# Kernel tuning notes

Measured on AMD Instinct MI355X. Metric: run time of the kernel, lower is better.

The kernel has to match this reference:

```python
import jax, jax.numpy as jnp
import numpy as np

SIZE = 4096
NB = 16            # nr_blocks_per_row
NDROP = 8          # nr_blocks_to_drop_per_row
BATCH = 8192
BLOCK = SIZE // NB # 256


def _block_mask():
    # latin_square(n): S[i,j] = ((i+j) mod n) + 1, values 1..n, each once per row/col
    i = np.arange(NB)
    S = ((i[:, None] + i[None, :]) % NB) + 1
    m = S > NDROP  # keep NB-NDROP blocks per row
    mask = np.repeat(np.repeat(m, BLOCK, axis=0), BLOCK, axis=1)
    return jnp.asarray(mask)  # [SIZE, SIZE] bool


def setup_inputs() -> dict:
    key = jax.random.key(0)
    kx, kw, kb = jax.random.split(key, 3)
    x = jax.random.normal(kx, (BATCH, SIZE), dtype=jnp.float32)
    # kaiming_normal_ default: fan_in mode, relu gain -> std = sqrt(2/fan_in)
    weight = jax.random.normal(kw, (SIZE, SIZE), dtype=jnp.float32) * jnp.sqrt(2.0 / SIZE)
    # uniform(-1,1) scaled by sqrt(1/size)
    bias = jax.random.uniform(kb, (SIZE,), minval=-1.0, maxval=1.0, dtype=jnp.float32) * jnp.sqrt(1.0 / SIZE)
    mask = _block_mask()
    return {"x": x, "weight": weight, "bias": bias, "mask": mask}


def reference(x, weight, bias, mask):
    # x @ (mask * weight).T + bias
    w = jnp.where(mask, weight, jnp.zeros((), dtype=weight.dtype))
    return x @ w.T + bias
```

## Files before the change

### kernel.cpp

```cpp
#include <hip/hip_runtime.h>
#include <hip/hip_bf16.h>
#include <stdint.h>


typedef __bf16 bf16x8 __attribute__((ext_vector_type(8)));
typedef float  f32x16 __attribute__((ext_vector_type(16)));

#define AS1 __attribute__((address_space(1)))
#define AS3 __attribute__((address_space(3)))

__device__ __forceinline__ void async_cp16(const void* g, void* l) {
  __builtin_amdgcn_global_load_lds((const AS1 void*)g, (AS3 void*)l, 16, 0, 0);
}

__device__ __forceinline__ uint32_t pack_bf16(float a, float b) {
  uint32_t ua = __float_as_uint(a);
  ua += 0x7fffu + ((ua >> 16) & 1u);
  uint32_t ub = __float_as_uint(b);
  ub += 0x7fffu + ((ub >> 16) & 1u);
  return (ua >> 16) | (ub & 0xffff0000u);
}

__global__ __launch_bounds__(256) void cvt_x(const float* __restrict__ x,
                                             uint2* __restrict__ xb) {
  const int t = threadIdx.x;
  const int b = blockIdx.x;
  const float4* p = (const float4*)(x + (size_t)b * 4096);
  uint2* o = xb + (size_t)b * 1024;
  float4 a0 = p[t];
  float4 a1 = p[t + 256];
  float4 a2 = p[t + 512];
  float4 a3 = p[t + 768];
  o[t]       = make_uint2(pack_bf16(a0.x, a0.y), pack_bf16(a0.z, a0.w));
  o[t + 256] = make_uint2(pack_bf16(a1.x, a1.y), pack_bf16(a1.z, a1.w));
  o[t + 512] = make_uint2(pack_bf16(a2.x, a2.y), pack_bf16(a2.z, a2.w));
  o[t + 768] = make_uint2(pack_bf16(a3.x, a3.y), pack_bf16(a3.z, a3.w));
}

__global__ __launch_bounds__(256) void cvt_w(const float* __restrict__ w,
                                             uint2* __restrict__ wb) {
  const int t = threadIdx.x;
  const int n = blockIdx.x;
  const int kstart = ((8 - (n >> 8)) & 15) << 8;
  const float* src = w + (size_t)n * 4096;
  uint2* dst = wb + (size_t)n * 512;
  float4 a0 = *(const float4*)(src + ((kstart + 4 * t) & 4095));
  float4 a1 = *(const float4*)(src + ((kstart + 1024 + 4 * t) & 4095));
  dst[t]       = make_uint2(pack_bf16(a0.x, a0.y), pack_bf16(a0.z, a0.w));
  dst[t + 256] = make_uint2(pack_bf16(a1.x, a1.y), pack_bf16(a1.z, a1.w));
}

__global__ __launch_bounds__(512, 2) void gemm_bs8(
    const uint16_t* __restrict__ X,
    const uint16_t* __restrict__ W,
    const float* __restrict__ bias,
    float* __restrict__ out) {
  __shared__ char L[131072];

  const int tid = threadIdx.x;
  const int lin = blockIdx.x;
  const int xcd = lin & 7;
  const int idx = lin >> 3;
  const int bm = idx >> 1;
  const int bn = (xcd << 1) + (idx & 1);
  const int m0 = bm << 8;
  const int n0 = bn << 8;
  const int kstart = ((8 - bn) & 15) << 8;

  const int trow = tid >> 3;
  const int chswz = (((tid & 7) ^ (trow & 7)) << 3);
  const uint16_t* Xa = X + (size_t)(m0 + trow) * 4096 + chswz;
  const uint16_t* Wa = W + (size_t)(n0 + trow) * 2048 + chswz;
  char* dA = L + tid * 16;
  char* dB = L + 32768 + tid * 16;

  auto stageA = [&](int buf, int s) {
    const int kb = (kstart + (s << 6)) & 4095;
    const uint16_t* p = Xa + kb;
    char* d = dA + (buf << 16);
#pragma unroll
    for (int c = 0; c < 4; ++c)
      async_cp16(p + (size_t)(c << 6) * 4096, d + (c << 13));
  };
  auto stageB = [&](int buf, int s) {
    const uint16_t* p = Wa + (s << 6);
    char* d = dB + (buf << 16);
#pragma unroll
    for (int c = 0; c < 4; ++c)
      async_cp16(p + (size_t)(c << 6) * 2048, d + (c << 13));
  };

  const int lane = tid & 63;
  const int wv = tid >> 6;
  const int wmh = wv >> 2;
  const int wnq = wv & 3;
  const int cl = lane & 31;
  const int g01 = lane >> 5;
  const int lx7 = lane & 7;
  int sl[4];
#pragma unroll
  for (int s = 0; s < 4; ++s) sl[s] = (((2 * s + g01) ^ lx7) << 4);
  const int aoff = (wmh * 128 + cl) * 128;
  const int boff = 32768 + (wnq * 64 + cl) * 128;

  f32x16 acc[4][2];
#pragma unroll
  for (int i = 0; i < 4; ++i)
#pragma unroll
    for (int j = 0; j < 2; ++j)
#pragma unroll
      for (int e = 0; e < 16; ++e) acc[i][j][e] = 0.f;

  bf16x8 av[4][4];
  bf16x8 bv[4];

#define VMW(N) asm volatile("s_waitcnt vmcnt(" #N ")" ::: "memory")

#define PHASE(BUFB, QN, DOA, WAITSTMT, STAGE)                                 \
  {                                                                           \
    if (DOA) {                                                                \
      _Pragma("unroll")                                                       \
      for (int i = 0; i < 4; ++i)                                             \
        _Pragma("unroll")                                                     \
        for (int s = 0; s < 4; ++s)                                           \
          av[i][s] = *(const bf16x8*)(L + (BUFB) + aoff + i * 4096 + sl[s]);  \
    }                                                                         \
    _Pragma("unroll")                                                         \
    for (int s = 0; s < 4; ++s)                                               \
      bv[s] = *(const bf16x8*)(L + (BUFB) + boff + (QN) * 4096 + sl[s]);      \
    STAGE;                                                                    \
    __builtin_amdgcn_s_barrier();                                             \
    asm volatile("s_waitcnt lgkmcnt(0)" ::: "memory");                        \
    __builtin_amdgcn_sched_barrier(0);                                        \
    __builtin_amdgcn_s_setprio(1);                                            \
    _Pragma("unroll")                                                         \
    for (int s = 0; s < 4; ++s)                                               \
      _Pragma("unroll")                                                       \
      for (int i = 0; i < 4; ++i)                                             \
        acc[i][QN] = __builtin_amdgcn_mfma_f32_32x32x16_bf16(                 \
            av[i][s], bv[s], acc[i][QN], 0, 0, 0);                            \
    __builtin_amdgcn_s_setprio(0);                                            \
    WAITSTMT;                                                                 \
    __builtin_amdgcn_s_barrier();                                             \
  }

  stageA(0, 0);
  stageB(0, 0);
  asm volatile("s_waitcnt vmcnt(0)" ::: "memory");
  __builtin_amdgcn_s_barrier();

  for (int t = 0; t < 31; ++t) {
    const int bufb = (t & 1) << 16;
    const int nb = (t & 1) ^ 1;
    PHASE(bufb, 0, 1, VMW(4), stageA(nb, t + 1));
    PHASE(bufb, 1, 0, VMW(2), stageB(nb, t + 1));
  }
  PHASE((1 << 16), 0, 1, VMW(0), (void)0);
  PHASE((1 << 16), 1, 0, (void)0, (void)0);
#undef PHASE
#undef VMW

  const int r4 = g01 << 2;
#pragma unroll
  for (int j = 0; j < 2; ++j) {
    const int c = n0 + wnq * 64 + (j << 5) + cl;
    const float bz = bias[c];
#pragma unroll
    for (int i = 0; i < 4; ++i) {
      const int rb = m0 + wmh * 128 + (i << 5) + r4;
#pragma unroll
      for (int reg = 0; reg < 16; ++reg) {
        const int r = rb + (reg & 3) + ((reg >> 2) << 3);
        out[(size_t)r * 4096 + c] = acc[i][j][reg] + bz;
      }
    }
  }
}

extern "C" void kernel_launch(void* const* d_in, const int* in_sizes, int n_in,
                              void* d_out, int out_size, void* d_ws, size_t ws_size,
                              hipStream_t stream) {
  const float* x = (const float*)d_in[0];
  const float* w = (const float*)d_in[1];
  const float* bias = (const float*)d_in[2];
  float* out = (float*)d_out;

  uint16_t* xb = (uint16_t*)d_ws;
  uint16_t* wb = xb + (size_t)8192 * 4096;

  hipLaunchKernelGGL(cvt_x, dim3(8192), dim3(256), 0, stream, x, (uint2*)xb);
  hipLaunchKernelGGL(cvt_w, dim3(4096), dim3(256), 0, stream, w, (uint2*)wb);

  hipLaunchKernelGGL(gemm_bs8, dim3(512), dim3(512), 0, stream,
                     xb, wb, bias, out);
}
```

Measured before the change: 440.7 us.

## Switch GEMM to four-stage K=32 async pipeline with one barrier per step

The GEMM main loop moves from a two-buffer K=64 schedule to a four-slot ring of K=32 stages that keeps three loads in flight, with a new LDS layout and swizzle sized for 64-byte rows. Each step reads A and B fragments once and issues all eight MFMAs. The extra barrier and explicit lgkmcnt wait per phase are dropped, so each step has a single barrier after the vmcnt wait. This aims to hide global-load latency better and cut synchronisation overhead, but it doubles the iteration count and leaves LDS reads to compiler-inserted waits, which may weaken the scheduling.

```diff
diff --git a/kernel.cpp b/kernel.cpp
--- a/kernel.cpp
+++ b/kernel.cpp
@@ -50,7 +50,7 @@
   dst[t + 256] = make_uint2(pack_bf16(a1.x, a1.y), pack_bf16(a1.z, a1.w));
 }
 
-__global__ __launch_bounds__(512, 2) void gemm_bs8(
+__global__ __launch_bounds__(512, 2) void gemm_dp(
     const uint16_t* __restrict__ X,
     const uint16_t* __restrict__ W,
     const float* __restrict__ bias,
@@ -67,27 +67,20 @@
   const int n0 = bn << 8;
   const int kstart = ((8 - bn) & 15) << 8;
 
-  const int trow = tid >> 3;
-  const int chswz = (((tid & 7) ^ (trow & 7)) << 3);
-  const uint16_t* Xa = X + (size_t)(m0 + trow) * 4096 + chswz;
-  const uint16_t* Wa = W + (size_t)(n0 + trow) * 2048 + chswz;
-  char* dA = L + tid * 16;
-  char* dB = L + 32768 + tid * 16;
+  const int swc = (((tid & 3) ^ ((tid >> 3) & 3)) << 3);
+  const int rowt = tid >> 2;
+  const uint16_t* XaT = X + (size_t)(m0 + rowt) * 4096 + swc;
+  const uint16_t* WaT = W + (size_t)(n0 + rowt) * 2048 + swc;
+  char* dst0 = L + tid * 16;
 
-  auto stageA = [&](int buf, int s) {
-    const int kb = (kstart + (s << 6)) & 4095;
-    const uint16_t* p = Xa + kb;
-    char* d = dA + (buf << 16);
-#pragma unroll
-    for (int c = 0; c < 4; ++c)
-      async_cp16(p + (size_t)(c << 6) * 4096, d + (c << 13));
-  };
-  auto stageB = [&](int buf, int s) {
-    const uint16_t* p = Wa + (s << 6);
-    char* d = dB + (buf << 16);
-#pragma unroll
-    for (int c = 0; c < 4; ++c)
-      async_cp16(p + (size_t)(c << 6) * 2048, d + (c << 13));
+  auto stage = [&](int sidx) {
+    const int kbA = (kstart + (sidx << 5)) & 4095;
+    const int kbB = sidx << 5;
+    char* base = dst0 + ((sidx & 3) << 15);
+    async_cp16(XaT + kbA, base);
+    async_cp16(XaT + 524288 + kbA, base + 8192);
+    async_cp16(WaT + kbB, base + 16384);
+    async_cp16(WaT + 262144 + kbB, base + 24576);
   };
 
   const int lane = tid & 63;
@@ -96,12 +89,12 @@
   const int wnq = wv & 3;
   const int cl = lane & 31;
   const int g01 = lane >> 5;
-  const int lx7 = lane & 7;
-  int sl[4];
+  const int rsw = (cl >> 1) & 3;
+  int sl[2];
 #pragma unroll
-  for (int s = 0; s < 4; ++s) sl[s] = (((2 * s + g01) ^ lx7) << 4);
-  const int aoff = (wmh * 128 + cl) * 128;
-  const int boff = 32768 + (wnq * 64 + cl) * 128;
+  for (int s = 0; s < 2; ++s) sl[s] = (((2 * s + g01) ^ rsw) << 4);
+  const int aoff = (wmh * 128 + cl) * 64;
+  const int boff = 16384 + (wnq * 64 + cl) * 64;
 
   f32x16 acc[4][2];
 #pragma unroll
@@ -111,53 +104,49 @@
 #pragma unroll
       for (int e = 0; e < 16; ++e) acc[i][j][e] = 0.f;
 
-  bf16x8 av[4][4];
-  bf16x8 bv[4];
-
 #define VMW(N) asm volatile("s_waitcnt vmcnt(" #N ")" ::: "memory")
 
-#define PHASE(BUFB, QN, DOA, WAITSTMT, STAGE)                                 \
+#define STEP(T, DOSTAGE, WAITSTMT, DOBAR)                                     \
   {                                                                           \
-    if (DOA) {                                                                \
+    const int bufb = ((T) & 3) << 15;                                         \
+    bf16x8 av[4][2], bv[2][2];                                                \
+    _Pragma("unroll")                                                         \
+    for (int i = 0; i < 4; ++i)                                               \
+      _Pragma("unroll")                                                       \
+      for (int s = 0; s < 2; ++s)                                             \
+        av[i][s] = *(const bf16x8*)(L + bufb + aoff + i * 2048 + sl[s]);      \
+    _Pragma("unroll")                                                         \
+    for (int j = 0; j < 2; ++j)                                               \
+      _Pragma("unroll")                                                       \
+      for (int s = 0; s < 2; ++s)                                             \
+        bv[j][s] = *(const bf16x8*)(L + bufb + boff + j * 2048 + sl[s]);      \
+    DOSTAGE;                                                                  \
+    __builtin_amdgcn_s_setprio(1);                                            \
+    _Pragma("unroll")                                                         \
+    for (int s = 0; s < 2; ++s)                                               \
       _Pragma("unroll")                                                       \
       for (int i = 0; i < 4; ++i)                                             \
         _Pragma("unroll")                                                     \
-        for (int s = 0; s < 4; ++s)                                           \
-          av[i][s] = *(const bf16x8*)(L + (BUFB) + aoff + i * 4096 + sl[s]);  \
-    }                                                                         \
-    _Pragma("unroll")                                                         \
-    for (int s = 0; s < 4; ++s)                                               \
-      bv[s] = *(const bf16x8*)(L + (BUFB) + boff + (QN) * 4096 + sl[s]);      \
-    STAGE;                                                                    \
-    __builtin_amdgcn_s_barrier();                                             \
-    asm volatile("s_waitcnt lgkmcnt(0)" ::: "memory");                        \
-    __builtin_amdgcn_sched_barrier(0);                                        \
-    __builtin_amdgcn_s_setprio(1);                                            \
-    _Pragma("unroll")                                                         \
-    for (int s = 0; s < 4; ++s)                                               \
-      _Pragma("unroll")                                                       \
-      for (int i = 0; i < 4; ++i)                                             \
-        acc[i][QN] = __builtin_amdgcn_mfma_f32_32x32x16_bf16(                 \
-            av[i][s], bv[s], acc[i][QN], 0, 0, 0);                            \
+        for (int j = 0; j < 2; ++j)                                           \
+          acc[i][j] = __builtin_amdgcn_mfma_f32_32x32x16_bf16(                \
+              av[i][s], bv[j][s], acc[i][j], 0, 0, 0);                        \
     __builtin_amdgcn_s_setprio(0);                                            \
     WAITSTMT;                                                                 \
-    __builtin_amdgcn_s_barrier();                                             \
+    if (DOBAR) __builtin_amdgcn_s_barrier();                                  \
   }
 
-  stageA(0, 0);
-  stageB(0, 0);
-  asm volatile("s_waitcnt vmcnt(0)" ::: "memory");
+  stage(0);
+  stage(1);
+  stage(2);
+  VMW(8);
   __builtin_amdgcn_s_barrier();
 
-  for (int t = 0; t < 31; ++t) {
-    const int bufb = (t & 1) << 16;
-    const int nb = (t & 1) ^ 1;
-    PHASE(bufb, 0, 1, VMW(4), stageA(nb, t + 1));
-    PHASE(bufb, 1, 0, VMW(2), stageB(nb, t + 1));
-  }
-  PHASE((1 << 16), 0, 1, VMW(0), (void)0);
-  PHASE((1 << 16), 1, 0, (void)0, (void)0);
-#undef PHASE
+  for (int t = 0; t < 61; ++t)
+    STEP(t, stage(t + 3), VMW(8), 1);
+  STEP(61, (void)0, VMW(4), 1);
+  STEP(62, (void)0, VMW(0), 1);
+  STEP(63, (void)0, (void)0, 0);
+#undef STEP
 #undef VMW
 
   const int r4 = g01 << 2;
@@ -191,6 +180,6 @@
   hipLaunchKernelGGL(cvt_x, dim3(8192), dim3(256), 0, stream, x, (uint2*)xb);
   hipLaunchKernelGGL(cvt_w, dim3(4096), dim3(256), 0, stream, w, (uint2*)wb);
 
-  hipLaunchKernelGGL(gemm_bs8, dim3(512), dim3(512), 0, stream,
+  hipLaunchKernelGGL(gemm_dp, dim3(512), dim3(512), 0, stream,
                      xb, wb, bias, out);
 }
```

Measured after the change: 429.0 us. 1.03x faster.
